# Kernel tuning notes

Hardware: AMD Instinct MI355X
Metric: run time of the kernel (lower is better)

The kernel has to match this reference:

```python
import jax, jax.numpy as jnp
import numpy as np

B, T, D, H, HS = 2, 256, 2048, 32, 64
LORA, DLORA, ST = 32, 64, 66  # maa lora rank, decay lora rank, state rows (2+HS)
EPS = 1e-5


def setup_inputs() -> dict:
    key = jax.random.key(0)
    ks = jax.random.split(key, 24)
    n = lambda k, sh, s=0.02: (jax.random.normal(k, sh, jnp.float32) * s)
    u = lambda k, sh: jax.random.uniform(k, sh, jnp.float32)
    return {
        "x": jax.random.normal(ks[0], (B, T, D), jnp.float32),
        "state": jax.random.normal(ks[1], (B, ST, D), jnp.float32) * 0.1,
        "ln1_w": jnp.ones((D,), jnp.float32),
        "ln1_b": jnp.zeros((D,), jnp.float32),
        "time_maa_x": u(ks[2], (D,)),
        "time_maa_w1": n(ks[3], (D, 5 * LORA)),
        "time_maa_w2": n(ks[4], (5, LORA, D)),
        "time_maa_k": u(ks[5], (D,)),
        "time_maa_w": u(ks[6], (D,)),
        "time_maa_v": u(ks[7], (D,)),
        "time_maa_r": u(ks[8], (D,)),
        "time_maa_g": u(ks[9], (D,)),
        "time_decay": n(ks[10], (D,), 0.5),
        "time_decay_w1": n(ks[11], (D, DLORA)),
        "time_decay_w2": n(ks[12], (DLORA, D)),
        "time_faaaa": n(ks[13], (H, HS, 1), 0.1),
        "receptance_weight": n(ks[14], (D, D)),
        "key_weight": n(ks[15], (D, D)),
        "value_weight": n(ks[16], (D, D)),
        "output_weight": n(ks[17], (D, D)),
        "gate_weight": n(ks[18], (D, D)),
        "lnx_w": jnp.ones((D,), jnp.float32),
        "lnx_b": jnp.zeros((D,), jnp.float32),
        "i": 0,
    }


def reference(x, state, ln1_w, ln1_b, time_maa_x, time_maa_w1, time_maa_w2,
              time_maa_k, time_maa_w, time_maa_v, time_maa_r, time_maa_g,
              time_decay, time_decay_w1, time_decay_w2, time_faaaa,
              receptance_weight, key_weight, value_weight, output_weight,
              gate_weight, lnx_w, lnx_b, i):
    # forward() early-returns time_mixing(ln1(x), state, i)
    mu = x.mean(-1, keepdims=True)
    var = ((x - mu) ** 2).mean(-1, keepdims=True)
    x = (x - mu) * jax.lax.rsqrt(var + EPS) * ln1_w + ln1_b

    i1 = (2 + HS) * i + 1
    # token shift: sx[t] = x[t-1] - x[t], with state row i1 as x[-1]
    sx = jnp.concatenate([state[:, i1][:, None] - x[:, :1], x[:, :-1] - x[:, 1:]], axis=1)

    xxx = x + sx * time_maa_x
    t5 = jnp.tanh(xxx @ time_maa_w1).reshape(B, T, 5, LORA)
    xxx5 = jnp.einsum('btfr,frd->btfd', t5, time_maa_w2)          # [B,T,5,D]
    maa = jnp.stack([time_maa_k, time_maa_w, time_maa_v, time_maa_r, time_maa_g])  # [5,D]
    x5 = x[:, :, None] + sx[:, :, None] * (maa + xxx5)            # [B,T,5,D]

    k = (x5[:, :, 0] @ key_weight.T).reshape(B, T, H, HS)
    w = jnp.exp(-jnp.exp(time_decay + jnp.tanh(x5[:, :, 1] @ time_decay_w1) @ time_decay_w2)).reshape(B, T, H, HS)
    v = (x5[:, :, 2] @ value_weight.T).reshape(B, T, H, HS)
    r = (x5[:, :, 3] @ receptance_weight.T).reshape(B, T, H, HS)
    g = jax.nn.silu(x5[:, :, 4] @ gate_weight.T)                  # [B,T,D]

    kv = jnp.einsum('bthi,bthj->bthij', k, v)                     # [B,T,H,HS,HS]
    prev0 = state[:, i1 + 1:i1 + 1 + HS].reshape(B, H, HS, HS)

    def step(prev, xs):
        kv_t, w_t = xs
        return kv_t + w_t[..., None] * prev, prev  # emit state BEFORE update

    _, state_s = jax.lax.scan(step, prev0,
                              (kv.transpose(1, 0, 2, 3, 4), w.transpose(1, 0, 2, 3)))
    state_s = state_s.transpose(1, 0, 2, 3, 4)                    # [B,T,H,HS,HS]

    wkv = time_faaaa * kv + state_s
    rwkv = jnp.einsum('bthj,bthjd->bthd', r, wkv)                 # [B,T,H,HS]

    # GroupNorm(num_groups=H) over each head's HS channels
    gm = rwkv.mean(-1, keepdims=True)
    gv = ((rwkv - gm) ** 2).mean(-1, keepdims=True)
    normed = (rwkv - gm) * jax.lax.rsqrt(gv + EPS)
    normed = normed * lnx_w.reshape(H, HS) + lnx_b.reshape(H, HS)
    normed = normed.reshape(B, T, D)

    return (normed * g) @ output_weight.T
```

## Files before the change

kernel.cpp:

```cpp
#include <hip/hip_runtime.h>
#include <hip/hip_bf16.h>

typedef unsigned short u16;
typedef __attribute__((ext_vector_type(4))) float f32x4;
typedef __attribute__((ext_vector_type(8))) short short8;
typedef __attribute__((ext_vector_type(4))) short bf16x4;

#define B_ 2
#define T_ 256
#define D_ 2048
#define H_ 32
#define HS_ 64
#define M_ 512
#define ST_ 66
#define EPS_ 1e-5f
#define NC_ 16
#define CL_ 16

__device__ __forceinline__ float bf2f(u16 u) {
    union { unsigned int i; float f; } c; c.i = ((unsigned int)u) << 16; return c.f;
}
__device__ __forceinline__ u16 f2bf(float f) {
    union { unsigned int i; float f; } c; c.f = f;
    unsigned int r = c.i + 0x7fffu + ((c.i >> 16) & 1u);
    return (u16)(r >> 16);
}
__device__ __forceinline__ u16 f2bf_hw(float f) {
    __hip_bfloat16 b = __float2bfloat16(f);
    return *reinterpret_cast<u16*>(&b);
}

__device__ __forceinline__ void gld16(const u16* g, u16* l) {
    __builtin_amdgcn_global_load_lds((const __attribute__((address_space(1))) void*)g,
                                     (__attribute__((address_space(3))) void*)l, 16, 0, 0);
}

__global__ __launch_bounds__(256) void ln_kernel(const float* __restrict__ x, const float* __restrict__ w,
                                                 const float* __restrict__ bias, float* __restrict__ xln)
{
    const int row = blockIdx.x;
    const float* xr = x + (size_t)row * D_;
    float* orow = xln + (size_t)row * D_;
    const int t = threadIdx.x;
    f32x4 a0 = *(const f32x4*)(xr + t * 8);
    f32x4 a1 = *(const f32x4*)(xr + t * 8 + 4);
    float s = 0.f, q = 0.f;
#pragma unroll
    for (int i = 0; i < 4; i++) { s += a0[i] + a1[i]; q += a0[i]*a0[i] + a1[i]*a1[i]; }
#pragma unroll
    for (int off = 1; off < 64; off <<= 1) { s += __shfl_xor(s, off, 64); q += __shfl_xor(q, off, 64); }
    __shared__ float ls[4], lq[4];
    const int wid = t >> 6, lane = t & 63;
    if (lane == 0) { ls[wid] = s; lq[wid] = q; }
    __syncthreads();
    s = ls[0] + ls[1] + ls[2] + ls[3];
    q = lq[0] + lq[1] + lq[2] + lq[3];
    const float mu = s * (1.f / D_);
    const float var = q * (1.f / D_) - mu * mu;
    const float rs = rsqrtf(var + EPS_);
#pragma unroll
    for (int i = 0; i < 8; i++) {
        int d = t * 8 + i;
        float f = (i < 4) ? a0[i] : a1[i - 4];
        orow[d] = (f - mu) * rs * w[d] + bias[d];
    }
}

__global__ __launch_bounds__(256) void shift_kernel(const float* __restrict__ xln, const float* __restrict__ state,
                                                    const float* __restrict__ maax, const int* __restrict__ ip,
                                                    float* __restrict__ sx, u16* __restrict__ xxxb)
{
    const size_t gid = (size_t)blockIdx.x * 256 + threadIdx.x;
    const size_t e = gid * 4;
    const int row = (int)(e >> 11);
    const int d = (int)(e & 2047);
    const int tt = row & (T_ - 1);
    const int b = row >> 8;
    const float* prev;
    if (tt == 0) prev = state + ((size_t)b * ST_ + (size_t)(66 * ip[0] + 1)) * D_ + d;
    else         prev = xln + e - D_;
    f32x4 p = *(const f32x4*)prev;
    f32x4 c = *(const f32x4*)(xln + e);
    f32x4 mx = *(const f32x4*)(maax + d);
    f32x4 sv;
    bf16x4 xv;
#pragma unroll
    for (int i = 0; i < 4; i++) { sv[i] = p[i] - c[i]; xv[i] = (short)f2bf(c[i] + sv[i] * mx[i]); }
    *(f32x4*)(sx + e) = sv;
    *(bf16x4*)(xxxb + e) = xv;
}

__global__ __launch_bounds__(256) void txp_kernel(const float* __restrict__ in, u16* __restrict__ out,
                                                  int K, int N)
{
    __shared__ float tile[32][33];
    const int k0 = blockIdx.x * 32, n0 = blockIdx.y * 32;
    const int c = threadIdx.x & 31, r8 = threadIdx.x >> 5;
#pragma unroll
    for (int i = 0; i < 4; i++) {
        int r = r8 + i * 8;
        tile[r][c] = in[(size_t)(k0 + r) * N + (n0 + c)];
    }
    __syncthreads();
#pragma unroll
    for (int i = 0; i < 4; i++) {
        int r = r8 + i * 8;
        out[(size_t)(n0 + r) * K + (k0 + c)] = f2bf(tile[c][r]);
    }
}

template<bool TANH>
__global__ __launch_bounds__(512) void wdot_kernel(const u16* __restrict__ A, const u16* __restrict__ Wt,
                                                   float* __restrict__ C, int N)
{
    const int gw = (int)((blockIdx.x * 512 + threadIdx.x) >> 6);
    const int lane = threadIdx.x & 63;
    const int m = gw / N, n = gw - m * N;
    const u16* a = A + (size_t)m * D_ + lane * 8;
    const u16* w = Wt + (size_t)n * D_ + lane * 8;
    float acc = 0.f;
#pragma unroll
    for (int i = 0; i < 4; i++) {
        short8 av = *(const short8*)(a + i * 512);
        short8 wv = *(const short8*)(w + i * 512);
#pragma unroll
        for (int j = 0; j < 8; j++)
            acc = fmaf(bf2f((u16)av[j]), bf2f((u16)wv[j]), acc);
    }
#pragma unroll
    for (int off = 1; off < 64; off <<= 1) acc += __shfl_xor(acc, off, 64);
    if (lane == 0) C[gw] = TANH ? tanhf(acc) : acc;
}

__global__ __launch_bounds__(256) void maa2_kernel(const float* __restrict__ t5, const float* __restrict__ w2,
                                                   const float* __restrict__ xln, const float* __restrict__ sxp,
                                                   const float* __restrict__ mk, const float* __restrict__ mw,
                                                   const float* __restrict__ mv, const float* __restrict__ mr,
                                                   const float* __restrict__ mg, u16* __restrict__ x5)
{
    const int gid = blockIdx.x * 256 + threadIdx.x;
    const int d = gid & (D_ - 1);
    const int mg4 = gid >> 11;
    const size_t m0 = (size_t)mg4 * 4;
    float xl[4], sv[4];
#pragma unroll
    for (int mm = 0; mm < 4; mm++) {
        const size_t e = (m0 + mm) * D_ + d;
        xl[mm] = xln[e];
        sv[mm] = sxp[e];
    }
    const float* t5b = t5 + m0 * 160;
#pragma unroll
    for (int f = 0; f < 5; f++) {
        const float* maa = (f == 0) ? mk : (f == 1) ? mw : (f == 2) ? mv : (f == 3) ? mr : mg;
        const float mf = maa[d];
        const float* w2f = w2 + (size_t)f * 32 * D_ + d;
        float a0 = 0, a1 = 0, a2 = 0, a3 = 0;
#pragma unroll 8
        for (int r = 0; r < 32; r++) {
            const float wv = w2f[(size_t)r * D_];
            a0 = fmaf(t5b[f * 32 + r], wv, a0);
            a1 = fmaf(t5b[160 + f * 32 + r], wv, a1);
            a2 = fmaf(t5b[320 + f * 32 + r], wv, a2);
            a3 = fmaf(t5b[480 + f * 32 + r], wv, a3);
        }
        const float accs[4] = {a0, a1, a2, a3};
#pragma unroll
        for (int mm = 0; mm < 4; mm++) {
            const size_t e = (m0 + mm) * D_ + d;
            x5[(size_t)f * M_ * D_ + e] = f2bf(xl[mm] + sv[mm] * (mf + accs[mm]));
        }
    }
}

__global__ __launch_bounds__(256) void decay2_kernel(const float* __restrict__ td, const float* __restrict__ dw2,
                                                     const float* __restrict__ tdec, float* __restrict__ wout)
{
    const int gid = blockIdx.x * 256 + threadIdx.x;
    const int d = gid & (D_ - 1);
    const int mg4 = gid >> 11;
    const float* wp = dw2 + d;
    const float* tb = td + (size_t)mg4 * 4 * 64;
    float a0 = 0, a1 = 0, a2 = 0, a3 = 0;
#pragma unroll 8
    for (int r = 0; r < 64; r++) {
        float wv = wp[(size_t)r * D_];
        a0 = fmaf(tb[r], wv, a0);
        a1 = fmaf(tb[64 + r], wv, a1);
        a2 = fmaf(tb[128 + r], wv, a2);
        a3 = fmaf(tb[192 + r], wv, a3);
    }
    const float base = tdec[d];
    const float accs[4] = {a0, a1, a2, a3};
#pragma unroll
    for (int mm = 0; mm < 4; mm++)
        wout[((size_t)mg4 * 4 + mm) * D_ + d] = expf(-expf(base + accs[mm]));
}

__device__ __forceinline__ void gemm2p_body(const u16* __restrict__ A, const float* __restrict__ Wf,
                                            float* __restrict__ C, int m0, int n0, int k0, int KC)
{
    __shared__ u16 As[2][128 * 32];
    __shared__ u16 Bs[2][64 * 32];
    const int tid = threadIdx.x;
    const int lane = tid & 63;
    const int wvd = tid >> 6;
    const int wm = (wvd >> 1) * 64;
    const int wn = (wvd & 1) * 32;

    f32x4 acc[4][2];
#pragma unroll
    for (int i = 0; i < 4; i++)
#pragma unroll
        for (int j = 0; j < 2; j++) { acc[i][j][0]=0.f; acc[i][j][1]=0.f; acc[i][j][2]=0.f; acc[i][j][3]=0.f; }

    const int srow = tid >> 2;
    const int schk = tid & 3;
    const u16* Ag = A + (size_t)(m0 + srow) * D_ + k0 + ((schk ^ (srow & 3)) << 3);
    const int ldst = tid * 8;

    const int br = srow;
    const float* Wg = Wf + (size_t)(n0 + br) * D_ + k0 + schk * 8;
    const int bdst = br * 32 + (((schk) ^ (br & 3)) << 3);

    const int fr = lane & 15;
    const int rchk = ((lane >> 4) ^ (fr & 3)) << 3;

    f32x4 xa0, xa1;
    f32x4 xb0, xb1;

#define LOADB_A(kt) { xa0 = *(const f32x4*)(Wg + (kt)); xa1 = *(const f32x4*)(Wg + (kt) + 4); }
#define LOADB_B(kt) { xb0 = *(const f32x4*)(Wg + (kt)); xb1 = *(const f32x4*)(Wg + (kt) + 4); }
#define STAGEA_(bb, kt)                                                           \
    {                                                                             \
        gld16(Ag + (kt), &As[bb][ldst]);                                          \
        gld16(Ag + (size_t)64 * D_ + (kt), &As[bb][2048 + ldst]);                 \
    }
#define WRITEB_(bb, r0, r1)                                                       \
    {                                                                             \
        short8 p0;                                                                \
        _Pragma("unroll")                                                         \
        for (int j = 0; j < 4; j++) {                                             \
            p0[j]     = (short)f2bf_hw(r0[j]);                                    \
            p0[j + 4] = (short)f2bf_hw(r1[j]);                                    \
        }                                                                         \
        *(short8*)&Bs[bb][bdst] = p0;                                             \
    }
#define MFMA_(bb)                                                                 \
    {                                                                             \
        short8 av[4], bv[2];                                                      \
        _Pragma("unroll")                                                         \
        for (int mi = 0; mi < 4; mi++)                                            \
            av[mi] = *(const short8*)&As[bb][(wm + mi * 16 + fr) * 32 + rchk];    \
        _Pragma("unroll")                                                         \
        for (int ni = 0; ni < 2; ni++)                                            \
            bv[ni] = *(const short8*)&Bs[bb][(wn + ni * 16 + fr) * 32 + rchk];    \
        _Pragma("unroll")                                                         \
        for (int mi = 0; mi < 4; mi++)                                            \
            _Pragma("unroll")                                                     \
            for (int ni = 0; ni < 2; ni++)                                        \
                acc[mi][ni] = __builtin_amdgcn_mfma_f32_16x16x32_bf16(av[mi], bv[ni], acc[mi][ni], 0, 0, 0); \
    }

    LOADB_A(0);
    STAGEA_(0, 0);
    for (int kt = 0; ; kt += 64) {
        {
            const bool m1 = kt + 32 < KC;
            if (m1) { LOADB_B(kt + 32); STAGEA_(1, kt + 32); }
            if (m1) asm volatile("s_waitcnt vmcnt(4)" ::: "memory");
            else    asm volatile("s_waitcnt vmcnt(0)" ::: "memory");
            WRITEB_(0, xa0, xa1);
            asm volatile("s_waitcnt lgkmcnt(0)" ::: "memory");
            __builtin_amdgcn_s_barrier();
            MFMA_(0);
            __builtin_amdgcn_s_barrier();
            if (!m1) break;
        }
        {
            const bool m2 = kt + 64 < KC;
            if (m2) { LOADB_A(kt + 64); STAGEA_(0, kt + 64); }
            if (m2) asm volatile("s_waitcnt vmcnt(4)" ::: "memory");
            else    asm volatile("s_waitcnt vmcnt(0)" ::: "memory");
            WRITEB_(1, xb0, xb1);
            asm volatile("s_waitcnt lgkmcnt(0)" ::: "memory");
            __builtin_amdgcn_s_barrier();
            MFMA_(1);
            __builtin_amdgcn_s_barrier();
            if (!m2) break;
        }
    }
#undef LOADB_A
#undef LOADB_B
#undef STAGEA_
#undef WRITEB_
#undef MFMA_
    const int cr = wm + (lane >> 4) * 4;
    const int cc = wn + fr;
#pragma unroll
    for (int mi = 0; mi < 4; mi++)
#pragma unroll
        for (int ni = 0; ni < 2; ni++)
#pragma unroll
            for (int j = 0; j < 4; j++)
                C[(size_t)(m0 + cr + mi * 16 + j) * D_ + (n0 + cc + ni * 16)] = acc[mi][ni][j];
}

__global__ __launch_bounds__(256) void gemm4g_kernel(const u16* __restrict__ x5, const float* __restrict__ Wk,
                                                     const float* __restrict__ Wv, const float* __restrict__ Wr,
                                                     const float* __restrict__ Wg, float* __restrict__ kvK,
                                                     float* __restrict__ kvV, float* __restrict__ kvR,
                                                     float* __restrict__ kvG, float* __restrict__ pp4)
{
    const int s  = blockIdx.z >> 1;
    const int ks = blockIdx.z & 1;
    const u16* A = x5 + (size_t)(s == 0 ? 0 : s + 1) * M_ * D_;
    const float* W = (s == 0) ? Wk : (s == 1) ? Wv : (s == 2) ? Wr : Wg;
    float* C = (ks == 0) ? ((s == 0) ? kvK : (s == 1) ? kvV : (s == 2) ? kvR : kvG)
                         : pp4 + (size_t)s * M_ * D_;
    gemm2p_body(A, W, C, blockIdx.y * 128, blockIdx.x * 64, ks * 1024, 1024);
}

__global__ __launch_bounds__(256) void add4g_kernel(float* __restrict__ dk, float* __restrict__ dv,
                                                    float* __restrict__ dr, float* __restrict__ dg,
                                                    const float* __restrict__ pp4)
{
    const int s = blockIdx.y;
    float* dst = (s == 0) ? dk : (s == 1) ? dv : (s == 2) ? dr : dg;
    const size_t e = ((size_t)blockIdx.x * 256 + threadIdx.x) * 4;
    f32x4 d = *(const f32x4*)(dst + e);
    f32x4 a = *(const f32x4*)(pp4 + (size_t)s * M_ * D_ + e);
#pragma unroll
    for (int i = 0; i < 4; i++) d[i] += a[i];
    *(f32x4*)(dst + e) = d;
}

__global__ __launch_bounds__(256) void gemm1g_kernel(const u16* __restrict__ y, const float* __restrict__ wo,
                                                     float* __restrict__ out, float* __restrict__ pp1)
{
    const int ks = blockIdx.z;
    float* C = (ks == 0) ? out : pp1 + (size_t)(ks - 1) * M_ * D_;
    gemm2p_body(y, wo, C, blockIdx.y * 128, blockIdx.x * 64, ks * 256, 256);
}

__global__ __launch_bounds__(256) void add7_kernel(float* __restrict__ dst, const float* __restrict__ pp1)
{
    const size_t e = ((size_t)blockIdx.x * 256 + threadIdx.x) * 4;
    const size_t MD = (size_t)M_ * D_;
    f32x4 d = *(const f32x4*)(dst + e);
#pragma unroll
    for (int i = 0; i < 7; i++) {
        f32x4 a = *(const f32x4*)(pp1 + (size_t)i * MD + e);
#pragma unroll
        for (int j = 0; j < 4; j++) d[j] += a[j];
    }
    *(f32x4*)(dst + e) = d;
}

__global__ __launch_bounds__(512) void rec1_kernel(const float* __restrict__ rB, const float* __restrict__ kB,
                                                   const float* __restrict__ wB, const float* __restrict__ vB,
                                                   const float* __restrict__ fa, float* __restrict__ rwkv,
                                                   float* __restrict__ CS, float* __restrict__ RP,
                                                   float* __restrict__ PC)
{
    const int bx = blockIdx.x;
    const int c  = bx & (NC_ - 1);
    const int bh = bx >> 4;
    const int h = bh & 31, b = bh >> 5;
    const int tid = threadIdx.x;
    const int wv = tid >> 6, lane = tid & 63;
    const int wg = wv >> 2;
    const int jb = lane >> 3, dsub = lane & 7;
    const int jbase = jb * 8;
    const int d0 = wg * 32 + (wv & 3) * 8 + dsub;

    __shared__ float stage[4][CL_][64];
    __shared__ float p2[CL_][8][64];
    __shared__ float p1[CL_][8];
    __shared__ float rpS[CL_ * 64];

    float S[8], pv[8], faj[8];
#pragma unroll
    for (int q = 0; q < 8; q++) { S[q] = 0.f; pv[q] = 1.f; faj[q] = fa[h * 64 + jbase + q]; }

    const size_t base = ((size_t)b * T_ * H_ + h) * HS_;
    const int t0 = c * CL_;
    const int arr = wv & 3;
    const float* mysrc = (arr == 0) ? rB : (arr == 1) ? kB : (arr == 2) ? wB : vB;
    const int ts0 = wg * 8 + (lane >> 4);
    const int sch = (lane & 15) * 4;
    const bool p1w = (wv == 0 && dsub == 0);

#pragma unroll
    for (int p = 0; p < 2; p++) {
        f32x4 v = *(const f32x4*)(mysrc + base + (size_t)(t0 + ts0 + p * 4) * (H_ * HS_) + sch);
        *(f32x4*)&stage[arr][ts0 + p * 4][sch] = v;
    }
    __syncthreads();

    f32x4 r0 = *(const f32x4*)&stage[0][0][jbase];
    f32x4 r1 = *(const f32x4*)&stage[0][0][jbase + 4];
    f32x4 k0 = *(const f32x4*)&stage[1][0][jbase];
    f32x4 k1 = *(const f32x4*)&stage[1][0][jbase + 4];
    f32x4 w0 = *(const f32x4*)&stage[2][0][jbase];
    f32x4 w1 = *(const f32x4*)&stage[2][0][jbase + 4];
    float vd = stage[3][0][d0];
#pragma unroll
    for (int ts = 0; ts < CL_; ++ts) {
        f32x4 nr0 = r0, nr1 = r1, nk0 = k0, nk1 = k1, nw0 = w0, nw1 = w1;
        float nvd = vd;
        if (ts + 1 < CL_) {
            nr0 = *(const f32x4*)&stage[0][ts + 1][jbase];
            nr1 = *(const f32x4*)&stage[0][ts + 1][jbase + 4];
            nk0 = *(const f32x4*)&stage[1][ts + 1][jbase];
            nk1 = *(const f32x4*)&stage[1][ts + 1][jbase + 4];
            nw0 = *(const f32x4*)&stage[2][ts + 1][jbase];
            nw1 = *(const f32x4*)&stage[2][ts + 1][jbase + 4];
            nvd = stage[3][ts + 1][d0];
        }
        float s1 = 0.f, s2 = 0.f;
#pragma unroll
        for (int q = 0; q < 4; q++) {
            s1 = fmaf(r0[q] * faj[q],     k0[q], s1);
            s1 = fmaf(r1[q] * faj[q + 4], k1[q], s1);
            s2 = fmaf(r0[q], S[q],     s2);
            s2 = fmaf(r1[q], S[q + 4], s2);
        }
        p2[ts][jb][d0 ^ (jb << 3)] = s2;
        if (p1w) {
            p1[ts][jb] = s1;
#pragma unroll
            for (int q = 0; q < 4; q++) {
                rpS[ts * 64 + jbase + q]     = r0[q] * pv[q];
                rpS[ts * 64 + jbase + 4 + q] = r1[q] * pv[q + 4];
            }
        }
#pragma unroll
        for (int q = 0; q < 4; q++) {
            pv[q]     *= w0[q];
            pv[q + 4] *= w1[q];
            S[q]       = fmaf(w0[q], S[q],     k0[q] * vd);
            S[q + 4]   = fmaf(w1[q], S[q + 4], k1[q] * vd);
        }
        r0 = nr0; r1 = nr1; k0 = nk0; k1 = nk1; w0 = nw0; w1 = nw1; vd = nvd;
    }
    __syncthreads();
#pragma unroll
    for (int p = 0; p < 2; p++) {
        const int ts = wv * 2 + p;
        f32x4 p1a = *(const f32x4*)&p1[ts][0];
        f32x4 p1b = *(const f32x4*)&p1[ts][4];
        float s1t = ((p1a[0] + p1a[1]) + (p1a[2] + p1a[3])) +
                    ((p1b[0] + p1b[1]) + (p1b[2] + p1b[3]));
        float s2t = 0.f;
#pragma unroll
        for (int j = 0; j < 8; j++) s2t += p2[ts][j][lane ^ (j << 3)];
        const float vvv = stage[3][ts][lane];
        rwkv[base + (size_t)(t0 + ts) * (H_ * HS_) + lane] = fmaf(vvv, s1t, s2t);
    }
    RP[(size_t)bx * (CL_ * 64) + tid]       = rpS[tid];
    RP[(size_t)bx * (CL_ * 64) + 512 + tid] = rpS[512 + tid];
#pragma unroll
    for (int q = 0; q < 8; q++)
        CS[(size_t)bx * 4096 + (size_t)(jbase + q) * 64 + d0] = S[q];
    if (p1w) {
#pragma unroll
        for (int q = 0; q < 8; q++)
            PC[(size_t)bx * 64 + jbase + q] = pv[q];
    }
}

__global__ __launch_bounds__(512) void rec2_kernel(const float* __restrict__ state, const int* __restrict__ ip,
                                                   float* __restrict__ CS, const float* __restrict__ PC)
{
    const int bh = blockIdx.x;
    const int b = bh >> 5, h = bh & 31;
    const int tid = threadIdx.x;
    const int o = tid * 8;
    const int jrow = tid >> 3;
    const float* Sp = state + (size_t)b * ST_ * D_ + (size_t)(66 * ip[0] + 2) * D_ + (size_t)h * HS_ * HS_;
    f32x4 c0 = *(const f32x4*)(Sp + o);
    f32x4 c1 = *(const f32x4*)(Sp + o + 4);
    for (int c = 0; c < NC_; ++c) {
        float* cs = CS + ((size_t)(bh * NC_ + c)) * 4096 + o;
        f32x4 l0 = *(const f32x4*)cs;
        f32x4 l1 = *(const f32x4*)(cs + 4);
        const float pc = PC[(size_t)(bh * NC_ + c) * 64 + jrow];
        f32x4 n0, n1;
#pragma unroll
        for (int i = 0; i < 4; i++) { n0[i] = fmaf(pc, c0[i], l0[i]); n1[i] = fmaf(pc, c1[i], l1[i]); }
        *(f32x4*)cs = c0;
        *(f32x4*)(cs + 4) = c1;
        c0 = n0; c1 = n1;
    }
}

__global__ __launch_bounds__(256) void rec3gn_kernel(const float* __restrict__ CS, const float* __restrict__ RP,
                                                     const float* __restrict__ rwkv, const float* __restrict__ gpre,
                                                     const float* __restrict__ lnxw, const float* __restrict__ lnxb,
                                                     u16* __restrict__ y)
{
    const int bx = blockIdx.x;
    const int c  = bx & (NC_ - 1);
    const int bh = bx >> 4;
    const int h = bh & 31, b = bh >> 5;
    const int tid = threadIdx.x;
    __shared__ float Ss[4096];
    __shared__ float rp[CL_ * 64];
#pragma unroll
    for (int i = 0; i < 4; i++)
        *(f32x4*)&Ss[tid * 4 + i * 1024] = *(const f32x4*)(CS + (size_t)bx * 4096 + tid * 4 + i * 1024);
    *(f32x4*)&rp[tid * 4] = *(const f32x4*)(RP + (size_t)bx * (CL_ * 64) + tid * 4);
    __syncthreads();
    const int tl = tid >> 4;
    const int d4 = (tid & 15) * 4;
    f32x4 acc; acc[0] = acc[1] = acc[2] = acc[3] = 0.f;
    const float* rpr = &rp[tl * 64];
#pragma unroll 16
    for (int j = 0; j < 64; ++j) {
        const float rv = rpr[j];
        const f32x4 sv = *(const f32x4*)&Ss[j * 64 + d4];
#pragma unroll
        for (int i = 0; i < 4; i++) acc[i] = fmaf(rv, sv[i], acc[i]);
    }
    const size_t base = ((size_t)b * T_ * H_ + h) * HS_;
    const size_t eb = base + (size_t)(c * CL_ + tl) * (H_ * HS_);
    const f32x4 cur = *(const f32x4*)(rwkv + eb + d4);
    f32x4 val;
#pragma unroll
    for (int i = 0; i < 4; i++) val[i] = cur[i] + acc[i];
    float s = 0.f, q = 0.f;
#pragma unroll
    for (int i = 0; i < 4; i++) { s += val[i]; q += val[i] * val[i]; }
#pragma unroll
    for (int off = 1; off < 16; off <<= 1) { s += __shfl_xor(s, off, 64); q += __shfl_xor(q, off, 64); }
    const float mu = s * (1.f / 64.f);
    const float var = q * (1.f / 64.f) - mu * mu;
    const float rs = rsqrtf(var + EPS_);
    bf16x4 yv;
#pragma unroll
    for (int i = 0; i < 4; i++) {
        const int hj = h * 64 + d4 + i;
        const float nrm = (val[i] - mu) * rs * lnxw[hj] + lnxb[hj];
        const float gp = gpre[eb + d4 + i];
        const float gv = gp / (1.f + expf(-gp));
        yv[i] = (short)f2bf(nrm * gv);
    }
    *(bf16x4*)(y + eb + d4) = yv;
}

extern "C" void kernel_launch(void* const* d_in, const int* in_sizes, int n_in,
                              void* d_out, int out_size, void* d_ws, size_t ws_size,
                              hipStream_t stream)
{
    const float* x     = (const float*)d_in[0];
    const float* state = (const float*)d_in[1];
    const float* ln1w  = (const float*)d_in[2];
    const float* ln1b  = (const float*)d_in[3];
    const float* maax  = (const float*)d_in[4];
    const float* w1    = (const float*)d_in[5];
    const float* w2    = (const float*)d_in[6];
    const float* maak  = (const float*)d_in[7];
    const float* maaw  = (const float*)d_in[8];
    const float* maav  = (const float*)d_in[9];
    const float* maar  = (const float*)d_in[10];
    const float* maag  = (const float*)d_in[11];
    const float* tdec  = (const float*)d_in[12];
    const float* dw1   = (const float*)d_in[13];
    const float* dw2   = (const float*)d_in[14];
    const float* fa    = (const float*)d_in[15];
    const float* wrec  = (const float*)d_in[16];
    const float* wkey  = (const float*)d_in[17];
    const float* wval  = (const float*)d_in[18];
    const float* wout  = (const float*)d_in[19];
    const float* wgate = (const float*)d_in[20];
    const float* lnxw  = (const float*)d_in[21];
    const float* lnxb  = (const float*)d_in[22];
    const int*   ip    = (const int*)d_in[23];

    char* ws = (char*)d_ws;
    const size_t MD = (size_t)M_ * D_;
    float* pp4  = (float*)(ws);
    float* CS   = (float*)(ws);
    float* RP   = (float*)(ws + ((size_t)16 << 20));
    float* PC   = (float*)(ws + ((size_t)20 << 20));
    float* pp1  = (float*)(ws);
    float* xln  = (float*)(ws + ((size_t)40 << 20));
    float* sx   = (float*)(ws + ((size_t)44 << 20));
    u16*   xxxb = (u16*)  (ws + ((size_t)48 << 20));
    u16*   w1t  = (u16*)  (ws + ((size_t)50 << 20));
    u16*   dw1t = (u16*)  (ws + ((size_t)51 << 20));
    float* t5   = (float*)(ws + ((size_t)52 << 20));
    float* td   = (float*)(ws + ((size_t)53 << 20));
    u16*   x5   = (u16*)  (ws + ((size_t)54 << 20));
    float* wdec = (float*)(ws + ((size_t)64 << 20));
    float* kvK  = (float*)(ws + ((size_t)40 << 20));
    float* kvV  = (float*)(ws + ((size_t)44 << 20));
    float* kvR  = (float*)(ws + ((size_t)48 << 20));
    float* kvG  = (float*)(ws + ((size_t)68 << 20));
    float* rwkv = (float*)(ws + ((size_t)72 << 20));
    u16*   y    = (u16*)  (ws + ((size_t)76 << 20));
    float* out  = (float*)d_out;

    hipLaunchKernelGGL(ln_kernel,     dim3(512),      dim3(256), 0, stream, x, ln1w, ln1b, xln);
    hipLaunchKernelGGL(shift_kernel,  dim3(1024),     dim3(256), 0, stream, xln, state, maax, ip, sx, xxxb);
    hipLaunchKernelGGL(txp_kernel,    dim3(64, 5),    dim3(256), 0, stream, w1, w1t, D_, 160);
    hipLaunchKernelGGL(txp_kernel,    dim3(64, 2),    dim3(256), 0, stream, dw1, dw1t, D_, 64);
    hipLaunchKernelGGL((wdot_kernel<true>), dim3(10240), dim3(512), 0, stream, xxxb, w1t, t5, 160);
    hipLaunchKernelGGL(maa2_kernel,   dim3(1024),     dim3(256), 0, stream, t5, w2, xln, sx, maak, maaw, maav, maar, maag, x5);
    hipLaunchKernelGGL((wdot_kernel<true>), dim3(4096), dim3(512), 0, stream, x5 + MD, dw1t, td, 64);
    hipLaunchKernelGGL(decay2_kernel, dim3(1024),     dim3(256), 0, stream, td, dw2, tdec, wdec);
    hipLaunchKernelGGL(gemm4g_kernel, dim3(32, 4, 8), dim3(256), 0, stream, x5, wkey, wval, wrec, wgate, kvK, kvV, kvR, kvG, pp4);
    hipLaunchKernelGGL(add4g_kernel,  dim3(1024, 4),  dim3(256), 0, stream, kvK, kvV, kvR, kvG, pp4);
    hipLaunchKernelGGL(rec1_kernel,   dim3(B_ * H_ * NC_), dim3(512), 0, stream, kvR, kvK, wdec, kvV, fa, rwkv, CS, RP, PC);
    hipLaunchKernelGGL(rec2_kernel,   dim3(B_ * H_),  dim3(512), 0, stream, state, ip, CS, PC);
    hipLaunchKernelGGL(rec3gn_kernel, dim3(B_ * H_ * NC_), dim3(256), 0, stream, CS, RP, rwkv, kvG, lnxw, lnxb, y);
    hipLaunchKernelGGL(gemm1g_kernel, dim3(32, 4, 8), dim3(256), 0, stream, y, wout, out, pp1);
    hipLaunchKernelGGL(add7_kernel,   dim3(1024),     dim3(256), 0, stream, out, pp1);

    (void)in_sizes; (void)n_in; (void)out_size; (void)ws_size;
}
```

Before: 195.9 us.

## Load GEMM B operand straight to registers, widen K tile, halve output split-K

The shared GEMM body no longer stages the fp32 weight tile through LDS. Each lane now loads its B fragment directly from global memory into registers, converts it to bf16 in registers and feeds MFMA, while the A tile in LDS grows to a K-chunk of 64 with an 8-way XOR swizzle. The output GEMM's split-K drops from 8 to 4, so the reduction kernel sums 3 partial buffers instead of 7. This removes the LDS writes, the lgkm wait and the partial-sum traffic, at the cost of more registers, possibly uncoalesced fp32 weight loads and fewer blocks for the output GEMM.

Measured after the change: 233.9 us. 19.4% more time.

```diff
diff --git a/kernel.cpp b/kernel.cpp
--- a/kernel.cpp
+++ b/kernel.cpp
@@ -200,8 +200,7 @@
 __device__ __forceinline__ void gemm2p_body(const u16* __restrict__ A, const float* __restrict__ Wf,
                                             float* __restrict__ C, int m0, int n0, int k0, int KC)
 {
-    __shared__ u16 As[2][128 * 32];
-    __shared__ u16 Bs[2][64 * 32];
+    __shared__ u16 As[2][128 * 64];
     const int tid = threadIdx.x;
     const int lane = tid & 63;
     const int wvd = tid >> 6;
@@ -214,88 +213,94 @@
 #pragma unroll
         for (int j = 0; j < 2; j++) { acc[i][j][0]=0.f; acc[i][j][1]=0.f; acc[i][j][2]=0.f; acc[i][j][3]=0.f; }
 
-    const int srow = tid >> 2;
-    const int schk = tid & 3;
-    const u16* Ag = A + (size_t)(m0 + srow) * D_ + k0 + ((schk ^ (srow & 3)) << 3);
+    const int srow = tid >> 3;
+    const int schk = tid & 7;
+    const u16* Ag = A + (size_t)(m0 + srow) * D_ + k0 + ((schk ^ (srow & 7)) << 3);
     const int ldst = tid * 8;
 
-    const int br = srow;
-    const float* Wg = Wf + (size_t)(n0 + br) * D_ + k0 + schk * 8;
-    const int bdst = br * 32 + (((schk) ^ (br & 3)) << 3);
-
     const int fr = lane & 15;
-    const int rchk = ((lane >> 4) ^ (fr & 3)) << 3;
-
-    f32x4 xa0, xa1;
-    f32x4 xb0, xb1;
-
-#define LOADB_A(kt) { xa0 = *(const f32x4*)(Wg + (kt)); xa1 = *(const f32x4*)(Wg + (kt) + 4); }
-#define LOADB_B(kt) { xb0 = *(const f32x4*)(Wg + (kt)); xb1 = *(const f32x4*)(Wg + (kt) + 4); }
+    const int gq = lane >> 4;
+
+    const float* Bg = Wf + (size_t)(n0 + wn + fr) * D_ + k0 + gq * 8;
+
+    f32x4 bc[8], bn[8];
+
+#define LOADB_(dst, kt)                                                           \
+    {                                                                             \
+        _Pragma("unroll")                                                         \
+        for (int ni = 0; ni < 2; ni++)                                            \
+        _Pragma("unroll")                                                         \
+        for (int kk = 0; kk < 2; kk++) {                                          \
+            const float* p = Bg + (size_t)(ni * 16) * D_ + (kt) + kk * 32;        \
+            dst[ni * 4 + kk * 2 + 0] = *(const f32x4*)p;                          \
+            dst[ni * 4 + kk * 2 + 1] = *(const f32x4*)(p + 4);                    \
+        }                                                                         \
+    }
 #define STAGEA_(bb, kt)                                                           \
     {                                                                             \
-        gld16(Ag + (kt), &As[bb][ldst]);                                          \
-        gld16(Ag + (size_t)64 * D_ + (kt), &As[bb][2048 + ldst]);                 \
-    }
-#define WRITEB_(bb, r0, r1)                                                       \
+        _Pragma("unroll")                                                         \
+        for (int i = 0; i < 4; i++)                                               \
+            gld16(Ag + (size_t)(i * 32) * D_ + (kt), &As[bb][i * 2048 + ldst]);   \
+    }
+#define MFMA_(bb, BR)                                                             \
     {                                                                             \
-        short8 p0;                                                                \
         _Pragma("unroll")                                                         \
-        for (int j = 0; j < 4; j++) {                                             \
-            p0[j]     = (short)f2bf_hw(r0[j]);                                    \
-            p0[j + 4] = (short)f2bf_hw(r1[j]);                                    \
-        }                                                                         \
-        *(short8*)&Bs[bb][bdst] = p0;                                             \
-    }
-#define MFMA_(bb)                                                                 \
-    {                                                                             \
-        short8 av[4], bv[2];                                                      \
-        _Pragma("unroll")                                                         \
-        for (int mi = 0; mi < 4; mi++)                                            \
-            av[mi] = *(const short8*)&As[bb][(wm + mi * 16 + fr) * 32 + rchk];    \
-        _Pragma("unroll")                                                         \
-        for (int ni = 0; ni < 2; ni++)                                            \
-            bv[ni] = *(const short8*)&Bs[bb][(wn + ni * 16 + fr) * 32 + rchk];    \
-        _Pragma("unroll")                                                         \
-        for (int mi = 0; mi < 4; mi++)                                            \
+        for (int kk2 = 0; kk2 < 2; kk2++) {                                       \
+            short8 av[4], bv[2];                                                  \
+            _Pragma("unroll")                                                     \
+            for (int mi = 0; mi < 4; mi++) {                                      \
+                const int row = wm + mi * 16 + fr;                                \
+                const int g = (gq + kk2 * 4) ^ (row & 7);                         \
+                av[mi] = *(const short8*)&As[bb][row * 64 + g * 8];               \
+            }                                                                     \
+            _Pragma("unroll")                                                     \
+            for (int ni = 0; ni < 2; ni++) {                                      \
+                const f32x4 lo = BR[ni * 4 + kk2 * 2];                            \
+                const f32x4 hi = BR[ni * 4 + kk2 * 2 + 1];                        \
+                short8 t;                                                         \
+                _Pragma("unroll")                                                 \
+                for (int j = 0; j < 4; j++) {                                     \
+                    t[j]     = (short)f2bf_hw(lo[j]);                             \
+                    t[j + 4] = (short)f2bf_hw(hi[j]);                             \
+                }                                                                 \
+                bv[ni] = t;                                                       \
+            }                                                                     \
+            _Pragma("unroll")                                                     \
+            for (int mi = 0; mi < 4; mi++)                                        \
             _Pragma("unroll")                                                     \
             for (int ni = 0; ni < 2; ni++)                                        \
                 acc[mi][ni] = __builtin_amdgcn_mfma_f32_16x16x32_bf16(av[mi], bv[ni], acc[mi][ni], 0, 0, 0); \
-    }
-
-    LOADB_A(0);
+        }                                                                         \
+    }
+
     STAGEA_(0, 0);
-    for (int kt = 0; ; kt += 64) {
+    LOADB_(bc, 0);
+    for (int kt = 0; ; kt += 128) {
         {
-            const bool m1 = kt + 32 < KC;
-            if (m1) { LOADB_B(kt + 32); STAGEA_(1, kt + 32); }
-            if (m1) asm volatile("s_waitcnt vmcnt(4)" ::: "memory");
+            const bool m1 = kt + 64 < KC;
+            if (m1) { STAGEA_(1, kt + 64); LOADB_(bn, kt + 64); }
+            if (m1) asm volatile("s_waitcnt vmcnt(12)" ::: "memory");
             else    asm volatile("s_waitcnt vmcnt(0)" ::: "memory");
-            WRITEB_(0, xa0, xa1);
-            asm volatile("s_waitcnt lgkmcnt(0)" ::: "memory");
             __builtin_amdgcn_s_barrier();
-            MFMA_(0);
+            MFMA_(0, bc);
             __builtin_amdgcn_s_barrier();
             if (!m1) break;
         }
         {
-            const bool m2 = kt + 64 < KC;
-            if (m2) { LOADB_A(kt + 64); STAGEA_(0, kt + 64); }
-            if (m2) asm volatile("s_waitcnt vmcnt(4)" ::: "memory");
+            const bool m2 = kt + 128 < KC;
+            if (m2) { STAGEA_(0, kt + 128); LOADB_(bc, kt + 128); }
+            if (m2) asm volatile("s_waitcnt vmcnt(12)" ::: "memory");
             else    asm volatile("s_waitcnt vmcnt(0)" ::: "memory");
-            WRITEB_(1, xb0, xb1);
-            asm volatile("s_waitcnt lgkmcnt(0)" ::: "memory");
             __builtin_amdgcn_s_barrier();
-            MFMA_(1);
+            MFMA_(1, bn);
             __builtin_amdgcn_s_barrier();
             if (!m2) break;
         }
     }
-#undef LOADB_A
-#undef LOADB_B
+#undef LOADB_
 #undef STAGEA_
-#undef WRITEB_
 #undef MFMA_
-    const int cr = wm + (lane >> 4) * 4;
+    const int cr = wm + gq * 4;
     const int cc = wn + fr;
 #pragma unroll
     for (int mi = 0; mi < 4; mi++)
@@ -340,16 +345,16 @@
 {
     const int ks = blockIdx.z;
     float* C = (ks == 0) ? out : pp1 + (size_t)(ks - 1) * M_ * D_;
-    gemm2p_body(y, wo, C, blockIdx.y * 128, blockIdx.x * 64, ks * 256, 256);
-}
-
-__global__ __launch_bounds__(256) void add7_kernel(float* __restrict__ dst, const float* __restrict__ pp1)
+    gemm2p_body(y, wo, C, blockIdx.y * 128, blockIdx.x * 64, ks * 512, 512);
+}
+
+__global__ __launch_bounds__(256) void add3_kernel(float* __restrict__ dst, const float* __restrict__ pp1)
 {
     const size_t e = ((size_t)blockIdx.x * 256 + threadIdx.x) * 4;
     const size_t MD = (size_t)M_ * D_;
     f32x4 d = *(const f32x4*)(dst + e);
 #pragma unroll
-    for (int i = 0; i < 7; i++) {
+    for (int i = 0; i < 3; i++) {
         f32x4 a = *(const f32x4*)(pp1 + (size_t)i * MD + e);
 #pragma unroll
         for (int j = 0; j < 4; j++) d[j] += a[j];
@@ -615,8 +620,8 @@
     hipLaunchKernelGGL(rec1_kernel,   dim3(B_ * H_ * NC_), dim3(512), 0, stream, kvR, kvK, wdec, kvV, fa, rwkv, CS, RP, PC);
     hipLaunchKernelGGL(rec2_kernel,   dim3(B_ * H_),  dim3(512), 0, stream, state, ip, CS, PC);
     hipLaunchKernelGGL(rec3gn_kernel, dim3(B_ * H_ * NC_), dim3(256), 0, stream, CS, RP, rwkv, kvG, lnxw, lnxb, y);
-    hipLaunchKernelGGL(gemm1g_kernel, dim3(32, 4, 8), dim3(256), 0, stream, y, wout, out, pp1);
-    hipLaunchKernelGGL(add7_kernel,   dim3(1024),     dim3(256), 0, stream, out, pp1);
+    hipLaunchKernelGGL(gemm1g_kernel, dim3(32, 4, 4), dim3(256), 0, stream, y, wout, out, pp1);
+    hipLaunchKernelGGL(add3_kernel,   dim3(1024),     dim3(256), 0, stream, out, pp1);
 
     (void)in_sizes; (void)n_in; (void)out_size; (void)ws_size;
 }
```

## Widen GEMM K-tile to 64 with 8 waves and cut split-K partial sums

Applied to the files above, without the earlier changes.

The shared GEMM body now stages 64-wide K tiles (up from 32) with an 8-chunk XOR swizzle and runs 512 threads, giving each of 8 waves a 32x32 sub-tile. The four projection GEMMs drop split-K entirely, which removes the separate add4g reduction pass and its partial-buffer traffic. The output projection goes from 8-way to 4-way split-K, so the final add sums 3 partials instead of 7. In exchange there are fewer blocks in flight, twice the LDS per block, and longer serial K loops per block.

New measurement: 174.9 us. 10.7% less time.

```diff
diff --git a/kernel.cpp b/kernel.cpp
--- a/kernel.cpp
+++ b/kernel.cpp
@@ -200,31 +200,30 @@
 __device__ __forceinline__ void gemm2p_body(const u16* __restrict__ A, const float* __restrict__ Wf,
                                             float* __restrict__ C, int m0, int n0, int k0, int KC)
 {
-    __shared__ u16 As[2][128 * 32];
-    __shared__ u16 Bs[2][64 * 32];
+    __shared__ u16 As[2][128 * 64];
+    __shared__ u16 Bs[2][64 * 64];
     const int tid = threadIdx.x;
     const int lane = tid & 63;
-    const int wvd = tid >> 6;
-    const int wm = (wvd >> 1) * 64;
-    const int wn = (wvd & 1) * 32;
-
-    f32x4 acc[4][2];
-#pragma unroll
-    for (int i = 0; i < 4; i++)
+    const int wvid = tid >> 6;
+    const int wm = (wvid >> 1) * 32;
+    const int wn = (wvid & 1) * 32;
+
+    f32x4 acc[2][2];
+#pragma unroll
+    for (int i = 0; i < 2; i++)
 #pragma unroll
         for (int j = 0; j < 2; j++) { acc[i][j][0]=0.f; acc[i][j][1]=0.f; acc[i][j][2]=0.f; acc[i][j][3]=0.f; }
 
-    const int srow = tid >> 2;
-    const int schk = tid & 3;
-    const u16* Ag = A + (size_t)(m0 + srow) * D_ + k0 + ((schk ^ (srow & 3)) << 3);
+    const int srow = tid >> 3;
+    const int schk = tid & 7;
+    const u16* Ag = A + (size_t)(m0 + srow) * D_ + k0 + ((schk ^ (srow & 7)) << 3);
     const int ldst = tid * 8;
 
-    const int br = srow;
-    const float* Wg = Wf + (size_t)(n0 + br) * D_ + k0 + schk * 8;
-    const int bdst = br * 32 + (((schk) ^ (br & 3)) << 3);
+    const float* Wg = Wf + (size_t)(n0 + srow) * D_ + k0 + schk * 8;
+    const int bdst = srow * 64 + ((schk ^ (srow & 7)) << 3);
 
     const int fr = lane & 15;
-    const int rchk = ((lane >> 4) ^ (fr & 3)) << 3;
+    const int gq = lane >> 4;
 
     f32x4 xa0, xa1;
     f32x4 xb0, xb1;
@@ -234,7 +233,7 @@
 #define STAGEA_(bb, kt)                                                           \
     {                                                                             \
         gld16(Ag + (kt), &As[bb][ldst]);                                          \
-        gld16(Ag + (size_t)64 * D_ + (kt), &As[bb][2048 + ldst]);                 \
+        gld16(Ag + (size_t)64 * D_ + (kt), &As[bb][4096 + ldst]);                 \
     }
 #define WRITEB_(bb, r0, r1)                                                       \
     {                                                                             \
@@ -248,26 +247,35 @@
     }
 #define MFMA_(bb)                                                                 \
     {                                                                             \
-        short8 av[4], bv[2];                                                      \
         _Pragma("unroll")                                                         \
-        for (int mi = 0; mi < 4; mi++)                                            \
-            av[mi] = *(const short8*)&As[bb][(wm + mi * 16 + fr) * 32 + rchk];    \
-        _Pragma("unroll")                                                         \
-        for (int ni = 0; ni < 2; ni++)                                            \
-            bv[ni] = *(const short8*)&Bs[bb][(wn + ni * 16 + fr) * 32 + rchk];    \
-        _Pragma("unroll")                                                         \
-        for (int mi = 0; mi < 4; mi++)                                            \
+        for (int kk = 0; kk < 2; kk++) {                                          \
+            short8 av[2], bv[2];                                                  \
+            _Pragma("unroll")                                                     \
+            for (int mi = 0; mi < 2; mi++) {                                      \
+                const int row = wm + mi * 16 + fr;                                \
+                const int g = (gq + kk * 4) ^ (row & 7);                          \
+                av[mi] = *(const short8*)&As[bb][row * 64 + g * 8];               \
+            }                                                                     \
+            _Pragma("unroll")                                                     \
+            for (int ni = 0; ni < 2; ni++) {                                      \
+                const int row = wn + ni * 16 + fr;                                \
+                const int g = (gq + kk * 4) ^ (row & 7);                          \
+                bv[ni] = *(const short8*)&Bs[bb][row * 64 + g * 8];               \
+            }                                                                     \
+            _Pragma("unroll")                                                     \
+            for (int mi = 0; mi < 2; mi++)                                        \
             _Pragma("unroll")                                                     \
             for (int ni = 0; ni < 2; ni++)                                        \
                 acc[mi][ni] = __builtin_amdgcn_mfma_f32_16x16x32_bf16(av[mi], bv[ni], acc[mi][ni], 0, 0, 0); \
+        }                                                                         \
     }
 
     LOADB_A(0);
     STAGEA_(0, 0);
-    for (int kt = 0; ; kt += 64) {
+    for (int kt = 0; ; kt += 128) {
         {
-            const bool m1 = kt + 32 < KC;
-            if (m1) { LOADB_B(kt + 32); STAGEA_(1, kt + 32); }
+            const bool m1 = kt + 64 < KC;
+            if (m1) { LOADB_B(kt + 64); STAGEA_(1, kt + 64); }
             if (m1) asm volatile("s_waitcnt vmcnt(4)" ::: "memory");
             else    asm volatile("s_waitcnt vmcnt(0)" ::: "memory");
             WRITEB_(0, xa0, xa1);
@@ -278,8 +286,8 @@
             if (!m1) break;
         }
         {
-            const bool m2 = kt + 64 < KC;
-            if (m2) { LOADB_A(kt + 64); STAGEA_(0, kt + 64); }
+            const bool m2 = kt + 128 < KC;
+            if (m2) { LOADB_A(kt + 128); STAGEA_(0, kt + 128); }
             if (m2) asm volatile("s_waitcnt vmcnt(4)" ::: "memory");
             else    asm volatile("s_waitcnt vmcnt(0)" ::: "memory");
             WRITEB_(1, xb0, xb1);
@@ -295,10 +303,10 @@
 #undef STAGEA_
 #undef WRITEB_
 #undef MFMA_
-    const int cr = wm + (lane >> 4) * 4;
+    const int cr = wm + gq * 4;
     const int cc = wn + fr;
 #pragma unroll
-    for (int mi = 0; mi < 4; mi++)
+    for (int mi = 0; mi < 2; mi++)
 #pragma unroll
         for (int ni = 0; ni < 2; ni++)
 #pragma unroll
@@ -306,50 +314,34 @@
                 C[(size_t)(m0 + cr + mi * 16 + j) * D_ + (n0 + cc + ni * 16)] = acc[mi][ni][j];
 }
 
-__global__ __launch_bounds__(256) void gemm4g_kernel(const u16* __restrict__ x5, const float* __restrict__ Wk,
+__global__ __launch_bounds__(512) void gemm4g_kernel(const u16* __restrict__ x5, const float* __restrict__ Wk,
                                                      const float* __restrict__ Wv, const float* __restrict__ Wr,
                                                      const float* __restrict__ Wg, float* __restrict__ kvK,
                                                      float* __restrict__ kvV, float* __restrict__ kvR,
-                                                     float* __restrict__ kvG, float* __restrict__ pp4)
-{
-    const int s  = blockIdx.z >> 1;
-    const int ks = blockIdx.z & 1;
+                                                     float* __restrict__ kvG)
+{
+    const int s = blockIdx.z;
     const u16* A = x5 + (size_t)(s == 0 ? 0 : s + 1) * M_ * D_;
     const float* W = (s == 0) ? Wk : (s == 1) ? Wv : (s == 2) ? Wr : Wg;
-    float* C = (ks == 0) ? ((s == 0) ? kvK : (s == 1) ? kvV : (s == 2) ? kvR : kvG)
-                         : pp4 + (size_t)s * M_ * D_;
-    gemm2p_body(A, W, C, blockIdx.y * 128, blockIdx.x * 64, ks * 1024, 1024);
-}
-
-__global__ __launch_bounds__(256) void add4g_kernel(float* __restrict__ dk, float* __restrict__ dv,
-                                                    float* __restrict__ dr, float* __restrict__ dg,
-                                                    const float* __restrict__ pp4)
-{
-    const int s = blockIdx.y;
-    float* dst = (s == 0) ? dk : (s == 1) ? dv : (s == 2) ? dr : dg;
-    const size_t e = ((size_t)blockIdx.x * 256 + threadIdx.x) * 4;
-    f32x4 d = *(const f32x4*)(dst + e);
-    f32x4 a = *(const f32x4*)(pp4 + (size_t)s * M_ * D_ + e);
-#pragma unroll
-    for (int i = 0; i < 4; i++) d[i] += a[i];
-    *(f32x4*)(dst + e) = d;
-}
-
-__global__ __launch_bounds__(256) void gemm1g_kernel(const u16* __restrict__ y, const float* __restrict__ wo,
+    float* C = (s == 0) ? kvK : (s == 1) ? kvV : (s == 2) ? kvR : kvG;
+    gemm2p_body(A, W, C, blockIdx.y * 128, blockIdx.x * 64, 0, D_);
+}
+
+__global__ __launch_bounds__(512) void gemm1g_kernel(const u16* __restrict__ y, const float* __restrict__ wo,
                                                      float* __restrict__ out, float* __restrict__ pp1)
 {
     const int ks = blockIdx.z;
     float* C = (ks == 0) ? out : pp1 + (size_t)(ks - 1) * M_ * D_;
-    gemm2p_body(y, wo, C, blockIdx.y * 128, blockIdx.x * 64, ks * 256, 256);
-}
-
-__global__ __launch_bounds__(256) void add7_kernel(float* __restrict__ dst, const float* __restrict__ pp1)
+    gemm2p_body(y, wo, C, blockIdx.y * 128, blockIdx.x * 64, ks * 512, 512);
+}
+
+__global__ __launch_bounds__(256) void add3_kernel(float* __restrict__ dst, const float* __restrict__ pp1)
 {
     const size_t e = ((size_t)blockIdx.x * 256 + threadIdx.x) * 4;
     const size_t MD = (size_t)M_ * D_;
     f32x4 d = *(const f32x4*)(dst + e);
 #pragma unroll
-    for (int i = 0; i < 7; i++) {
+    for (int i = 0; i < 3; i++) {
         f32x4 a = *(const f32x4*)(pp1 + (size_t)i * MD + e);
 #pragma unroll
         for (int j = 0; j < 4; j++) d[j] += a[j];
@@ -580,7 +572,6 @@
 
     char* ws = (char*)d_ws;
     const size_t MD = (size_t)M_ * D_;
-    float* pp4  = (float*)(ws);
     float* CS   = (float*)(ws);
     float* RP   = (float*)(ws + ((size_t)16 << 20));
     float* PC   = (float*)(ws + ((size_t)20 << 20));
@@ -610,13 +601,12 @@
     hipLaunchKernelGGL(maa2_kernel,   dim3(1024),     dim3(256), 0, stream, t5, w2, xln, sx, maak, maaw, maav, maar, maag, x5);
     hipLaunchKernelGGL((wdot_kernel<true>), dim3(4096), dim3(512), 0, stream, x5 + MD, dw1t, td, 64);
     hipLaunchKernelGGL(decay2_kernel, dim3(1024),     dim3(256), 0, stream, td, dw2, tdec, wdec);
-    hipLaunchKernelGGL(gemm4g_kernel, dim3(32, 4, 8), dim3(256), 0, stream, x5, wkey, wval, wrec, wgate, kvK, kvV, kvR, kvG, pp4);
-    hipLaunchKernelGGL(add4g_kernel,  dim3(1024, 4),  dim3(256), 0, stream, kvK, kvV, kvR, kvG, pp4);
+    hipLaunchKernelGGL(gemm4g_kernel, dim3(32, 4, 4), dim3(512), 0, stream, x5, wkey, wval, wrec, wgate, kvK, kvV, kvR, kvG);
     hipLaunchKernelGGL(rec1_kernel,   dim3(B_ * H_ * NC_), dim3(512), 0, stream, kvR, kvK, wdec, kvV, fa, rwkv, CS, RP, PC);
     hipLaunchKernelGGL(rec2_kernel,   dim3(B_ * H_),  dim3(512), 0, stream, state, ip, CS, PC);
     hipLaunchKernelGGL(rec3gn_kernel, dim3(B_ * H_ * NC_), dim3(256), 0, stream, CS, RP, rwkv, kvG, lnxw, lnxb, y);
-    hipLaunchKernelGGL(gemm1g_kernel, dim3(32, 4, 8), dim3(256), 0, stream, y, wout, out, pp1);
-    hipLaunchKernelGGL(add7_kernel,   dim3(1024),     dim3(256), 0, stream, out, pp1);
+    hipLaunchKernelGGL(gemm1g_kernel, dim3(32, 4, 4), dim3(512), 0, stream, y, wout, out, pp1);
+    hipLaunchKernelGGL(add3_kernel,   dim3(1024),     dim3(256), 0, stream, out, pp1);
 
     (void)in_sizes; (void)n_in; (void)out_size; (void)ws_size;
 }
```
